# Optimization experiments

Measured on AMD Instinct MI355X. Metric: run time of the kernel, lower is better.

## Reference

```python
import jax, jax.numpy as jnp
import numpy as np

N_HEADS = 32
N_KV = 8
HEAD_DIM = 128
EPS = 1e-5

def _rope(t, fr, fi):
    # t: [b,s,h,hd] -> pairs [b,s,h,hd/2,2]; fr/fi: [s,hd/2]
    tp = t.astype(jnp.float32).reshape(*t.shape[:-1], HEAD_DIM // 2, 2)
    a, b = tp[..., 0], tp[..., 1]
    fr = fr[None, :, None, :]
    fi = fi[None, :, None, :]
    out = jnp.stack([a * fr - b * fi, a * fi + b * fr], axis=-1)
    return out.reshape(t.shape).astype(t.dtype)

def _rmsnorm(t):
    tf = t.astype(jnp.float32)
    return (tf * jax.lax.rsqrt(jnp.mean(tf * tf, axis=-1, keepdims=True) + EPS)).astype(t.dtype)

def setup_inputs() -> dict:
    key = jax.random.key(0)
    ks = jax.random.split(key, 5)
    b, s, dim = 1, 2048, 4096
    x = jax.random.normal(ks[0], (b, s, dim), dtype=jnp.float32) * 0.02
    wq = jax.random.normal(ks[1], (dim, dim), dtype=jnp.float32) * 0.02
    wk = jax.random.normal(ks[2], (N_KV * HEAD_DIM, dim), dtype=jnp.float32) * 0.02
    wv = jax.random.normal(ks[3], (N_KV * HEAD_DIM, dim), dtype=jnp.float32) * 0.02
    wo = jax.random.normal(ks[4], (dim, dim), dtype=jnp.float32) * 0.02
    # RoPE freqs, llama-style theta=10000
    inv = 1.0 / (10000.0 ** (np.arange(0, HEAD_DIM, 2, dtype=np.float32) / HEAD_DIM))
    ang = np.outer(np.arange(s, dtype=np.float32), inv)  # [s, hd/2]
    freqs_cis = jnp.asarray(np.stack([np.cos(ang), np.sin(ang)], axis=-1))  # [s, hd/2, 2]
    # causal additive mask
    mask = jnp.where(jnp.tril(jnp.ones((s, s), dtype=bool)), 0.0, -1e30).astype(jnp.float32)
    return {"x": x, "wq": wq, "wk": wk, "wv": wv, "wo": wo,
            "freqs_cis": freqs_cis, "mask": mask, "start_pos": 0}

def reference(x, wq, wk, wv, wo, freqs_cis, mask, start_pos):
    b, s, dim = x.shape
    n_rep = N_HEADS // N_KV
    xq = jnp.einsum('bsd,ed->bse', x, wq).reshape(b, s, N_HEADS, HEAD_DIM)
    xk = jnp.einsum('bsd,ed->bse', x, wk).reshape(b, s, N_KV, HEAD_DIM)
    xv = jnp.einsum('bsd,ed->bse', x, wv).reshape(b, s, N_KV, HEAD_DIM)
    fr, fi = freqs_cis[..., 0], freqs_cis[..., 1]
    xq = _rope(xq, fr, fi)
    xk = _rope(xk, fr, fi)
    xq = _rmsnorm(xq)
    xk = _rmsnorm(xk)
    # start_pos=0 prefill: KV cache write/read is identity on xk/xv
    q = xq.transpose(0, 2, 1, 3).reshape(b, N_KV, n_rep, s, HEAD_DIM)  # grouped query heads
    k = xk.transpose(0, 2, 1, 3)  # [b, n_kv, s, hd]
    v = xv.transpose(0, 2, 1, 3)
    scores = jnp.einsum('bkrsd,bktd->bkrst', q, k) / np.sqrt(HEAD_DIM)
    scores = scores + mask[None, None, None, :, :]
    probs = jax.nn.softmax(scores, axis=-1)
    o = jnp.einsum('bkrst,bktd->bkrsd', probs, v)
    o = o.reshape(b, N_HEADS, s, HEAD_DIM).transpose(0, 2, 1, 3).reshape(b, s, dim)
    return jnp.einsum('bse,de->bsd', o, wo)
```

## Files before the change

kernel.cpp:

```cpp
#include <hip/hip_runtime.h>
#include <hip/hip_bf16.h>
#include <cstdint>
#include <cstddef>

using u16 = unsigned short;
using u32 = unsigned int;
using u64 = unsigned long long;

typedef __attribute__((ext_vector_type(8))) __bf16 bf16x8;
typedef __attribute__((ext_vector_type(4))) float f32x4;
typedef __attribute__((ext_vector_type(2))) float f32x2;
typedef __attribute__((ext_vector_type(4))) u32 u32x4;

typedef const __attribute__((address_space(1))) void* gas_ptr;
typedef __attribute__((address_space(3))) void* las_ptr;

__device__ __forceinline__ void async_cp16(const void* g, void* l) {
  __builtin_amdgcn_global_load_lds((gas_ptr)g, (las_ptr)l, 16, 0, 0);
}

__device__ __forceinline__ float bf2f(u16 u) {
  u32 v = ((u32)u) << 16;
  return __builtin_bit_cast(float, v);
}
__device__ __forceinline__ u16 f2bf(float f) {
  u32 v = __builtin_bit_cast(u32, f);
  u32 r = (v + 0x7fffu + ((v >> 16) & 1u)) >> 16;
  return (u16)r;
}

__device__ __forceinline__ f32x4 mfma16(bf16x8 a, bf16x8 b, f32x4 c) {
  return __builtin_amdgcn_mfma_f32_16x16x32_bf16(a, b, c, 0, 0, 0);
}

__global__ __launch_bounds__(256) void cvt4(const float* __restrict__ x,
                                            const float* __restrict__ wq,
                                            const float* __restrict__ wk,
                                            const float* __restrict__ wv,
                                            u16* __restrict__ xb,
                                            u16* __restrict__ wqkv) {
  const int B0 = 1048576;
  const int B1 = B0 + 2097152;
  const int B2 = B1 + 524288;
  const int B3 = B2 + 524288;
  int i = blockIdx.x * blockDim.x + threadIdx.x;
  int stride = gridDim.x * blockDim.x;
  for (; i < B3; i += stride) {
    const float* src; u16* dst; int j;
    if (i < B0)      { src = x;  dst = xb;                           j = i; }
    else if (i < B1) { src = wq; dst = wqkv;                         j = i - B0; }
    else if (i < B2) { src = wk; dst = wqkv + (size_t)4096 * 4096;   j = i - B1; }
    else             { src = wv; dst = wqkv + (size_t)5120 * 4096;   j = i - B2; }
    const float4* p = (const float4*)(src + (size_t)j * 8);
    float4 a = p[0], b = p[1];
    union { u16 us[8]; u32x4 v; } o;
    o.us[0] = f2bf(a.x); o.us[1] = f2bf(a.y); o.us[2] = f2bf(a.z); o.us[3] = f2bf(a.w);
    o.us[4] = f2bf(b.x); o.us[5] = f2bf(b.y); o.us[6] = f2bf(b.z); o.us[7] = f2bf(b.w);
    *(u32x4*)(dst + (size_t)j * 8) = o.v;
  }
}

__global__ __launch_bounds__(512, 2) void gemm256(const u16* __restrict__ A,
                                                  const u16* __restrict__ B,
                                                  int M, int N, int K,
                                                  u16* __restrict__ qh,
                                                  u16* __restrict__ khh,
                                                  u16* __restrict__ vt,
                                                  const float* __restrict__ freqs) {
  __shared__ __align__(16) u16 As[2][16384];
  __shared__ __align__(16) u16 Bs[2][16384];
  const int tid = threadIdx.x;
  const int wave = tid >> 6, lane = tid & 63;
  const int quad = lane >> 4, c16 = lane & 15;
  const int wr = wave >> 2, wc = wave & 3;

  const int mb = M >> 8;
  const int nb = N >> 8;
  const int per_xcd_n = nb >> 3;
  const int xcd = blockIdx.x & 7, lid = blockIdx.x >> 3;
  const int m_t = lid % mb, n_local = lid / mb;
  const int m0 = m_t * 256, n0 = (xcd * per_xcd_n + n_local) * 256;

  const u16* Ab = A + (size_t)m0 * K;
  const u16* Bb = B + (size_t)n0 * K;

  f32x4 acc[8][4] = {};

  auto stageA = [&](int k0, int ks, int b) __attribute__((always_inline)) {
#pragma unroll
    for (int i = 0; i < 2; ++i) {
      int n = tid + 512 * i;
      int row = n >> 2;
      int col = k0 + ks * 32 + (((n & 3) ^ (row & 3)) * 8);
      async_cp16(Ab + (size_t)row * K + col, &As[b][ks * 8192 + n * 8]);
    }
  };
  auto stageB = [&](int k0, int ks, int b) __attribute__((always_inline)) {
#pragma unroll
    for (int i = 0; i < 2; ++i) {
      int n = tid + 512 * i;
      int row = n >> 2;
      int col = k0 + ks * 32 + (((n & 3) ^ (row & 3)) * 8);
      async_cp16(Bb + (size_t)row * K + col, &Bs[b][ks * 8192 + n * 8]);
    }
  };

  auto phase_compute = [&](int b, int ks) __attribute__((always_inline)) {
    bf16x8 af[8], bf[4];
    const u16* Abase = &As[b][ks * 8192];
    const u16* Bbase = &Bs[b][ks * 8192];
#pragma unroll
    for (int mt = 0; mt < 8; ++mt) {
      int row = wr * 128 + mt * 16 + c16;
      af[mt] = *(const bf16x8*)(Abase + row * 32 + ((quad ^ (row & 3)) * 8));
    }
#pragma unroll
    for (int nt = 0; nt < 4; ++nt) {
      int row = wc * 64 + nt * 16 + c16;
      bf[nt] = *(const bf16x8*)(Bbase + row * 32 + ((quad ^ (row & 3)) * 8));
    }
    __builtin_amdgcn_s_setprio(1);
#pragma unroll
    for (int mt = 0; mt < 8; ++mt)
#pragma unroll
      for (int nt = 0; nt < 4; ++nt)
        acc[mt][nt] = mfma16(af[mt], bf[nt], acc[mt][nt]);
    __builtin_amdgcn_s_setprio(0);
  };

  const int nk = K >> 6;
  stageA(0, 0, 0);  stageB(0, 0, 0);
  stageA(0, 1, 0);  stageB(0, 1, 0);
  stageA(64, 0, 1); stageB(64, 0, 1);

#pragma unroll 1
  for (int t = 0; t < nk; ++t) {
    const int b = t & 1;
    const int k0 = t << 6;
    if (t < nk - 1) asm volatile("s_waitcnt vmcnt(8)" ::: "memory");
    else            asm volatile("s_waitcnt vmcnt(4)" ::: "memory");
    __builtin_amdgcn_s_barrier();
    __builtin_amdgcn_sched_barrier(0);
    if (t + 1 < nk) { stageA(k0 + 64, 1, b ^ 1); stageB(k0 + 64, 1, b ^ 1); }
    phase_compute(b, 0);
    if (t < nk - 1) asm volatile("s_waitcnt vmcnt(8)" ::: "memory");
    else            asm volatile("s_waitcnt vmcnt(0)" ::: "memory");
    __builtin_amdgcn_s_barrier();
    __builtin_amdgcn_sched_barrier(0);
    if (t + 2 < nk) { stageA(k0 + 128, 0, b); stageB(k0 + 128, 0, b); }
    phase_compute(b, 1);
  }

  __syncthreads();
  float* sums = (float*)&As[0][0];
  if (n0 < 5120) {
    float ss_arr[8][4];
    const int dbase = (wc & 1) * 64;
#pragma unroll
    for (int mt = 0; mt < 8; ++mt) {
#pragma unroll
      for (int r = 0; r < 4; ++r) {
        int s = m0 + wr * 128 + mt * 16 + quad * 4 + r;
        const float* fb = freqs + (size_t)s * 128;
        float ssv = 0.0f;
#pragma unroll
        for (int nt = 0; nt < 4; ++nt) {
          int d = dbase + nt * 16 + c16;
          float v = acc[mt][nt][r];
          float p = __shfl_xor(v, 1, 64);
          f32x2 ff = *(const f32x2*)(fb + (d & ~1));
          float res = (c16 & 1) ? fmaf(v, ff.x, p * ff.y)
                                : fmaf(v, ff.x, -p * ff.y);
          acc[mt][nt][r] = res;
          ssv = fmaf(res, res, ssv);
        }
#pragma unroll
        for (int m = 1; m < 16; m <<= 1) ssv += __shfl_xor(ssv, m, 64);
        ss_arr[mt][r] = ssv;
      }
    }
    if (c16 == 0) {
#pragma unroll
      for (int mt = 0; mt < 8; ++mt)
#pragma unroll
        for (int r = 0; r < 4; ++r)
          sums[wc * 256 + wr * 128 + mt * 16 + quad * 4 + r] = ss_arr[mt][r];
    }
    __syncthreads();
    const int head_col = n0 + wc * 64;
    u16* outb = (head_col < 4096)
                    ? (qh + (size_t)(head_col >> 7) * M * 128)
                    : (khh + (size_t)((head_col - 4096) >> 7) * M * 128);
#pragma unroll
    for (int mt = 0; mt < 8; ++mt) {
#pragma unroll
      for (int r = 0; r < 4; ++r) {
        int rl = wr * 128 + mt * 16 + quad * 4 + r;
        float tot = ss_arr[mt][r] + sums[(wc ^ 1) * 256 + rl];
        float scl = rsqrtf(tot * (1.0f / 128.0f) + 1e-5f);
        int s = m0 + rl;
#pragma unroll
        for (int nt = 0; nt < 4; ++nt)
          outb[(size_t)s * 128 + dbase + nt * 16 + c16] = f2bf(acc[mt][nt][r] * scl);
      }
    }
  } else {
#pragma unroll
    for (int mt = 0; mt < 8; ++mt) {
#pragma unroll
      for (int nt = 0; nt < 4; ++nt) {
        int dv = (n0 - 5120) + wc * 64 + nt * 16 + c16;
        int s0 = m0 + wr * 128 + mt * 16 + quad * 4;
        union { u16 us[4]; u64 v; } pk;
#pragma unroll
        for (int r = 0; r < 4; ++r) pk.us[r] = f2bf(acc[mt][nt][r]);
        *(u64*)(vt + (size_t)dv * M + s0) = pk.v;
      }
    }
  }
}

__global__ __launch_bounds__(256, 3) void gemm_out(const u16* __restrict__ A,
                                                   const u16* __restrict__ B,
                                                   float* __restrict__ C,
                                                   int M, int N, int K) {
  __shared__ __align__(16) u16 As[128 * 64];
  __shared__ __align__(16) u16 Bs[128 * 64];
  const int tid = threadIdx.x;
  const int wave = tid >> 6, lane = tid & 63;
  const int quad = lane >> 4, c16 = lane & 15;

  const int mb = M >> 7, nb = N >> 7;
  const int per_xcd_n = nb >> 3;
  const int xcd = blockIdx.x & 7, lid = blockIdx.x >> 3;
  const int m_t = lid % mb, n_local = lid / mb;
  const int m0 = m_t * 128, n0 = (xcd * per_xcd_n + n_local) * 128;

  const int wm = (wave & 1) * 64, wn = (wave >> 1) * 64;

  f32x4 acc[4][4] = {};

  const u16* Ab = A + (size_t)m0 * K;
  const u16* Bb = B + (size_t)n0 * K;

  for (int k0 = 0; k0 < K; k0 += 64) {
    __syncthreads();
#pragma unroll
    for (int i = 0; i < 4; ++i) {
      int idx = tid + 256 * i;
      int row = idx >> 3, sg = (idx & 7) ^ (row & 7);
      async_cp16(Ab + (size_t)row * K + k0 + sg * 8, As + (size_t)idx * 8);
    }
#pragma unroll
    for (int i = 0; i < 4; ++i) {
      int idx = tid + 256 * i;
      int row = idx >> 3, sg = (idx & 7) ^ (row & 7);
      async_cp16(Bb + (size_t)row * K + k0 + sg * 8, Bs + (size_t)idx * 8);
    }
    asm volatile("s_waitcnt vmcnt(0)" ::: "memory");
    __syncthreads();

    bf16x8 af[4][2], bfr[4][2];
#pragma unroll
    for (int mt = 0; mt < 4; ++mt) {
      int row = wm + mt * 16 + c16;
#pragma unroll
      for (int c = 0; c < 2; ++c)
        af[mt][c] = *(const bf16x8*)(As + row * 64 + (((c * 4 + quad) ^ (row & 7)) * 8));
    }
#pragma unroll
    for (int nt = 0; nt < 4; ++nt) {
      int row = wn + nt * 16 + c16;
#pragma unroll
      for (int c = 0; c < 2; ++c)
        bfr[nt][c] = *(const bf16x8*)(Bs + row * 64 + (((c * 4 + quad) ^ (row & 7)) * 8));
    }
#pragma unroll
    for (int c = 0; c < 2; ++c)
#pragma unroll
      for (int mt = 0; mt < 4; ++mt)
#pragma unroll
        for (int nt = 0; nt < 4; ++nt)
          acc[mt][nt] = mfma16(af[mt][c], bfr[nt][c], acc[mt][nt]);
  }

#pragma unroll
  for (int mt = 0; mt < 4; ++mt) {
#pragma unroll
    for (int nt = 0; nt < 4; ++nt) {
#pragma unroll
      for (int r = 0; r < 4; ++r) {
        int gm = m0 + wm + mt * 16 + quad * 4 + r;
        int gn = n0 + wn + nt * 16 + c16;
        C[(size_t)gm * N + gn] = acc[mt][nt][r];
      }
    }
  }
}

#define SEQ 2048
__global__ __launch_bounds__(512, 2) void attn(const u16* __restrict__ Q,
                                               const u16* __restrict__ Kh,
                                               const u16* __restrict__ VT,
                                               u16* __restrict__ O,
                                               const float* __restrict__ wo,
                                               u16* __restrict__ wob) {
  __shared__ __align__(16) u16 Ks[2][64 * 128];
  __shared__ __align__(16) u16 Vs[2][128 * 64];
  __shared__ __align__(16) u16 Ps[8][32 * 64];
  const int tid = threadIdx.x;
  const int wave = tid >> 6, lane = tid & 63;
  const int quad = lane >> 4, c16 = lane & 15;
  const int bid = blockIdx.x;
  const int hk = bid & 7;
  const int rest = bid >> 3;
  const int hq = rest & 3;
  const int p = rest >> 2;
  const int h = hk * 4 + hq;

  const int wl = wave & 3, grp = wave >> 2;
  const int qt = grp ? p : (15 - p);
  const int q0w = qt * 128 + wl * 32;
  const int kend = (15 - p) * 128 + 128;

  const float sc = 0.12751743f;
  const float B = 16.5f;
  const u16* Kb = Kh + (size_t)hk * SEQ * 128;
  const u16* Vb = VT + (size_t)hk * 128 * SEQ;

  auto stage = [&](int t0, int b) __attribute__((always_inline)) {
#pragma unroll
    for (int i = 0; i < 2; ++i) {
      int idx = tid + 512 * i;
      int row = idx >> 4, sg = (idx & 15) ^ (row & 7);
      async_cp16(Kb + (size_t)(t0 + row) * 128 + sg * 8, &Ks[b][(size_t)idx * 8]);
    }
#pragma unroll
    for (int i = 0; i < 2; ++i) {
      int idx = tid + 512 * i;
      int row = idx >> 3, sg = (idx & 7) ^ (row & 7);
      async_cp16(Vb + (size_t)row * SEQ + t0 + sg * 8, &Vs[b][(size_t)idx * 8]);
    }
  };

  bf16x8 qfr[2][4];
  const u16* qbase = Q + (size_t)h * SEQ * 128;
#pragma unroll
  for (int g = 0; g < 2; ++g)
#pragma unroll
    for (int c = 0; c < 4; ++c)
      qfr[g][c] =
          *(const bf16x8*)(qbase + (size_t)(q0w + g * 16 + c16) * 128 + c * 32 + quad * 8);

  f32x4 o_acc[2][8] = {};
  float lsum[2][4] = {};

  stage(0, 0);

#pragma unroll 1
  for (int t0 = 0; t0 < kend; t0 += 64) {
    const int cur = (t0 >> 6) & 1;
    asm volatile("s_waitcnt vmcnt(0)" ::: "memory");
    __syncthreads();
    if (t0 + 64 < kend) stage(t0 + 64, cur ^ 1);

    if (t0 < q0w + 32) {
      f32x4 sa[2][4] = {};
      __builtin_amdgcn_s_setprio(1);
#pragma unroll
      for (int ct = 0; ct < 4; ++ct) {
        int t = ct * 16 + c16;
        int tbase = t * 128;
        int tsw = t & 7;
#pragma unroll
        for (int c = 0; c < 4; ++c) {
          bf16x8 kf = *(const bf16x8*)(&Ks[cur][tbase + (((c * 4 + quad) ^ tsw) * 8)]);
          sa[0][ct] = mfma16(qfr[0][c], kf, sa[0][ct]);
          sa[1][ct] = mfma16(qfr[1][c], kf, sa[1][ct]);
        }
      }
      __builtin_amdgcn_s_setprio(0);

      const bool diag = (t0 + 64 > q0w);
      auto soft = [&](bool masked) __attribute__((always_inline)) {
#pragma unroll
        for (int g = 0; g < 2; ++g) {
#pragma unroll
          for (int r = 0; r < 4; ++r) {
            int row = g * 16 + quad * 4 + r;
            int row_q = q0w + row;
            int rbase = row * 64;
            int rsw = row & 7;
#pragma unroll
            for (int ct = 0; ct < 4; ++ct) {
              float s = sa[g][ct][r];
              float arg = fmaf(s, sc, -B);
              if (masked) {
                int t_idx = t0 + ct * 16 + c16;
                arg = (t_idx <= row_q) ? arg : -1.0e30f;
              }
              float pe = exp2f(arg);
              lsum[g][r] += pe;
              u32 pb = (__builtin_bit_cast(u32, pe) + 0x8000u) >> 16;
              Ps[wave][rbase + (((ct * 2 + (c16 >> 3)) ^ rsw) * 8) + (c16 & 7)] = (u16)pb;
            }
          }
        }
      };
      if (diag) soft(true); else soft(false);
      asm volatile("s_waitcnt lgkmcnt(0)" ::: "memory");

      __builtin_amdgcn_s_setprio(1);
#pragma unroll
      for (int tc = 0; tc < 2; ++tc) {
        bf16x8 pf[2];
#pragma unroll
        for (int g = 0; g < 2; ++g) {
          int prow = g * 16 + c16;
          pf[g] = *(const bf16x8*)(&Ps[wave][prow * 64 + (((tc * 4 + quad) ^ (prow & 7)) * 8)]);
        }
#pragma unroll
        for (int nt = 0; nt < 8; ++nt) {
          int dl = nt * 16 + c16;
          bf16x8 vf = *(const bf16x8*)(&Vs[cur][dl * 64 + (((tc * 4 + quad) ^ (dl & 7)) * 8)]);
          o_acc[0][nt] = mfma16(pf[0], vf, o_acc[0][nt]);
          o_acc[1][nt] = mfma16(pf[1], vf, o_acc[1][nt]);
        }
      }
      __builtin_amdgcn_s_setprio(0);
    }
  }

#pragma unroll
  for (int g = 0; g < 2; ++g) {
#pragma unroll
    for (int r = 0; r < 4; ++r) {
      float l = lsum[g][r];
#pragma unroll
      for (int m = 1; m < 16; m <<= 1) l += __shfl_xor(l, m, 64);
      float inv = 1.0f / l;
      int s_idx = q0w + g * 16 + quad * 4 + r;
      u16* ob = O + (size_t)s_idx * 4096 + (size_t)h * 128;
#pragma unroll
      for (int nt = 0; nt < 8; ++nt) ob[nt * 16 + c16] = f2bf(o_acc[g][nt][r] * inv);
    }
  }

  {
    const int UNIT = 2341;
    const int N8 = 2097152;
    int su = 16 * p * (p - 1) + (bid & 31) * p;
    int i = su * UNIT + tid;
    int end = su * UNIT + p * UNIT;
    if (end > N8) end = N8;
    for (; i < end; i += 512) {
      const float4* src = (const float4*)(wo + (size_t)i * 8);
      float4 a = src[0], b = src[1];
      union { u16 us[8]; u32x4 v; } o;
      o.us[0] = f2bf(a.x); o.us[1] = f2bf(a.y); o.us[2] = f2bf(a.z); o.us[3] = f2bf(a.w);
      o.us[4] = f2bf(b.x); o.us[5] = f2bf(b.y); o.us[6] = f2bf(b.z); o.us[7] = f2bf(b.w);
      *(u32x4*)(wob + (size_t)i * 8) = o.v;
    }
  }
}

extern "C" void kernel_launch(void* const* d_in, const int* in_sizes, int n_in,
                              void* d_out, int out_size, void* d_ws, size_t ws_size,
                              hipStream_t stream) {
  const float* x  = (const float*)d_in[0];
  const float* wq = (const float*)d_in[1];
  const float* wk = (const float*)d_in[2];
  const float* wv = (const float*)d_in[3];
  const float* wo = (const float*)d_in[4];
  const float* fr = (const float*)d_in[5];
  float* out = (float*)d_out;

  const size_t S = 2048, D = 4096, KV = 1024, NQKV = D + 2 * KV;
  u16* p = (u16*)d_ws;
  u16* xb   = p; p += S * D;
  u16* wqkv = p; p += NQKV * D;
  u16* qh   = p; p += S * D;
  u16* khh  = p; p += S * KV;
  u16* vt   = p; p += KV * S;
  u16* ob   = p; p += S * D;
  u16* wob = wqkv;

  cvt4<<<dim3(2048), dim3(256), 0, stream>>>(x, wq, wk, wv, xb, wqkv);

  gemm256<<<dim3((S / 256) * (NQKV / 256)), dim3(512), 0, stream>>>(
      xb, wqkv, (int)S, (int)NQKV, (int)D, qh, khh, vt, fr);

  attn<<<dim3(256), dim3(512), 0, stream>>>(qh, khh, vt, ob, wo, wob);

  gemm_out<<<dim3((S / 128) * (D / 128)), dim3(256), 0, stream>>>(
      ob, wob, out, (int)S, (int)D, (int)D);
}
```

Baseline: 490.9 us.

## Restructure GEMM mainloop into full-tile staging with four half-M compute phases

Staging the 256x64 A/B k-tile now happens in one shot, with a 64-element-wide row layout and an 8-way XOR swizzle. Before, each tile was split into two 32-wide halves staged at different points. Each k-tile is consumed in four phases covering two k-halves and two m-halves, with a barrier after each phase. The phases use smaller A fragment register sets and reuse B fragments between m-halves, which is meant to reduce register pressure and interleave LDS reads with MFMA. The cost is more barriers per iteration and a shallower prefetch depth (one tile ahead instead of one and a half).

```diff
diff --git a/kernel.cpp b/kernel.cpp
--- a/kernel.cpp
+++ b/kernel.cpp
@@ -86,69 +86,74 @@
 
   f32x4 acc[8][4] = {};
 
-  auto stageA = [&](int k0, int ks, int b) __attribute__((always_inline)) {
-#pragma unroll
-    for (int i = 0; i < 2; ++i) {
-      int n = tid + 512 * i;
-      int row = n >> 2;
-      int col = k0 + ks * 32 + (((n & 3) ^ (row & 3)) * 8);
-      async_cp16(Ab + (size_t)row * K + col, &As[b][ks * 8192 + n * 8]);
+  const int atg = wc * 64 + lane;
+  const int bh = wc >> 1;
+  const int btg = (((wr << 1) | (wc & 1)) << 6) + lane;
+
+  auto stage_tile = [&](int k0, int b) __attribute__((always_inline)) {
+#pragma unroll
+    for (int j = 0; j < 4; ++j) {
+      int idx = atg + 256 * j;
+      int rl = idx >> 3;
+      int row = wr * 128 + rl;
+      int sg = (idx & 7) ^ (row & 7);
+      async_cp16(Ab + (size_t)row * K + k0 + sg * 8, &As[b][wr * 8192 + idx * 8]);
+    }
+#pragma unroll
+    for (int j = 0; j < 4; ++j) {
+      int idx = btg + 256 * j;
+      int rl = idx >> 3;
+      int row = bh * 128 + rl;
+      int sg = (idx & 7) ^ (row & 7);
+      async_cp16(Bb + (size_t)row * K + k0 + sg * 8, &Bs[b][bh * 8192 + idx * 8]);
     }
   };
-  auto stageB = [&](int k0, int ks, int b) __attribute__((always_inline)) {
-#pragma unroll
-    for (int i = 0; i < 2; ++i) {
-      int n = tid + 512 * i;
-      int row = n >> 2;
-      int col = k0 + ks * 32 + (((n & 3) ^ (row & 3)) * 8);
-      async_cp16(Bb + (size_t)row * K + col, &Bs[b][ks * 8192 + n * 8]);
-    }
+
+  bf16x8 bfr[4];
+  auto phase = [&](int b, int ks, int mh, bool loadB) __attribute__((always_inline)) {
+    bf16x8 af[4];
+    if (loadB) {
+#pragma unroll
+      for (int nt = 0; nt < 4; ++nt) {
+        int row = wc * 64 + nt * 16 + c16;
+        bfr[nt] = *(const bf16x8*)(&Bs[b][row * 64 + (((ks * 4 + quad) ^ (row & 7)) * 8)]);
+      }
+    }
+#pragma unroll
+    for (int mt = 0; mt < 4; ++mt) {
+      int row = wr * 128 + (mh * 4 + mt) * 16 + c16;
+      af[mt] = *(const bf16x8*)(&As[b][row * 64 + (((ks * 4 + quad) ^ (row & 7)) * 8)]);
+    }
+    asm volatile("s_waitcnt lgkmcnt(0)" ::: "memory");
+    __builtin_amdgcn_sched_barrier(0);
+    __builtin_amdgcn_s_setprio(1);
+#pragma unroll
+    for (int mt = 0; mt < 4; ++mt)
+#pragma unroll
+      for (int nt = 0; nt < 4; ++nt)
+        acc[mh * 4 + mt][nt] = mfma16(af[mt], bfr[nt], acc[mh * 4 + mt][nt]);
+    __builtin_amdgcn_s_setprio(0);
+    __builtin_amdgcn_s_barrier();
   };
 
-  auto phase_compute = [&](int b, int ks) __attribute__((always_inline)) {
-    bf16x8 af[8], bf[4];
-    const u16* Abase = &As[b][ks * 8192];
-    const u16* Bbase = &Bs[b][ks * 8192];
-#pragma unroll
-    for (int mt = 0; mt < 8; ++mt) {
-      int row = wr * 128 + mt * 16 + c16;
-      af[mt] = *(const bf16x8*)(Abase + row * 32 + ((quad ^ (row & 3)) * 8));
-    }
-#pragma unroll
-    for (int nt = 0; nt < 4; ++nt) {
-      int row = wc * 64 + nt * 16 + c16;
-      bf[nt] = *(const bf16x8*)(Bbase + row * 32 + ((quad ^ (row & 3)) * 8));
-    }
-    __builtin_amdgcn_s_setprio(1);
-#pragma unroll
-    for (int mt = 0; mt < 8; ++mt)
-#pragma unroll
-      for (int nt = 0; nt < 4; ++nt)
-        acc[mt][nt] = mfma16(af[mt], bf[nt], acc[mt][nt]);
-    __builtin_amdgcn_s_setprio(0);
-  };
-
   const int nk = K >> 6;
-  stageA(0, 0, 0);  stageB(0, 0, 0);
-  stageA(0, 1, 0);  stageB(0, 1, 0);
-  stageA(64, 0, 1); stageB(64, 0, 1);
+  stage_tile(0, 0);
 
 #pragma unroll 1
   for (int t = 0; t < nk; ++t) {
     const int b = t & 1;
     const int k0 = t << 6;
-    if (t < nk - 1) asm volatile("s_waitcnt vmcnt(8)" ::: "memory");
-    else            asm volatile("s_waitcnt vmcnt(4)" ::: "memory");
+    if (t + 1 < nk) {
+      stage_tile(k0 + 64, b ^ 1);
+      asm volatile("s_waitcnt vmcnt(8)" ::: "memory");
+    } else {
+      asm volatile("s_waitcnt vmcnt(0)" ::: "memory");
+    }
     __builtin_amdgcn_s_barrier();
-    __builtin_amdgcn_sched_barrier(0);
-    if (t + 1 < nk) { stageA(k0 + 64, 1, b ^ 1); stageB(k0 + 64, 1, b ^ 1); }
-    phase_compute(b, 0);
-    if (t < nk - 1) asm volatile("s_waitcnt vmcnt(8)" ::: "memory");
-    else            asm volatile("s_waitcnt vmcnt(0)" ::: "memory");
-    __builtin_amdgcn_s_barrier();
-    __builtin_amdgcn_sched_barrier(0);
-    if (t + 2 < nk) { stageA(k0 + 128, 0, b); stageB(k0 + 128, 0, b); }
-    phase_compute(b, 1);
+    phase(b, 0, 0, true);
+    phase(b, 0, 1, false);
+    phase(b, 1, 0, true);
+    phase(b, 1, 1, false);
   }
 
   __syncthreads();
```

Result: no change. 496.0 us (+1.0%).
